# Kernel tuning notes

Measured on AMD Instinct MI355X. Metric: run time of the kernel, lower is better.

Reference implementation:

```python
import jax, jax.numpy as jnp
import numpy as np

N, E, H, R, C = 20000, 640000, 256, 10, 7
B, MAXLEN = 64, 110


def setup_inputs() -> dict:
    key = jax.random.key(0)
    ks = jax.random.split(key, 12)
    return {
        "speaker": jax.random.randint(ks[0], (N,), 0, 2),
        "x": jax.random.normal(ks[1], (N, H), dtype=jnp.float32),
        "edge_index": jax.random.randint(ks[2], (2, E), 0, N),
        "edge_norm": jax.random.uniform(ks[3], (E,), dtype=jnp.float32),
        "edge_type": jax.random.randint(ks[4], (E,), 0, R),
        "seq_lengths": jax.random.randint(ks[5], (B,), 1, MAXLEN),
        "umask": jnp.ones((B, MAXLEN), dtype=jnp.float32),
        "w1": jax.random.normal(ks[6], (R, H, H), dtype=jnp.float32) * 0.02,
        "w2": jax.random.normal(ks[7], (R, H, H), dtype=jnp.float32) * 0.02,
        "lin_W": jax.random.normal(ks[8], (2 * H, H), dtype=jnp.float32) * 0.02,
        "lin_b": jnp.zeros((H,), dtype=jnp.float32),
        "fc_W": jax.random.normal(ks[9], (H, C), dtype=jnp.float32) * 0.02,
        "fc_b": jnp.zeros((C,), dtype=jnp.float32),
    }


def gnn_layer(x, w, edge_index, edge_type, edge_norm):
    # PyG MessagePassing with flow='target_to_source', aggr='mean':
    #   x_j = x[edge_index[1]], aggregate at i = edge_index[0]
    i, j = edge_index[0], edge_index[1]
    # per-edge msg = x_j @ w[edge_type]; compute as relation-batched GEMM
    xw = jnp.einsum('nd,rdo->rno', x, w)          # [R, N, H]
    msgs = xw[edge_type, j] * edge_norm[:, None]   # [E, H]
    sums = jax.ops.segment_sum(msgs, i, num_segments=x.shape[0])
    cnt = jax.ops.segment_sum(jnp.ones_like(edge_norm), i, num_segments=x.shape[0])
    return sums / jnp.maximum(cnt, 1.0)[:, None]   # scatter-mean (0 for isolated nodes)


def reference(speaker, x, edge_index, edge_norm, edge_type, seq_lengths, umask,
              w1, w2, lin_W, lin_b, fc_W, fc_b):
    en = edge_norm * 2.0  # forward passes edge_norm * 2
    # both GNN layers are type 'GGCN' -> update() returns aggr_out (GRU path is dead)
    out1 = jax.nn.sigmoid(gnn_layer(x, w1, edge_index, edge_type, en))  # dropout = eval identity
    out2 = gnn_layer(out1, w2, edge_index, edge_type, en)
    emotions = jnp.concatenate([x, out2], axis=1)            # [N, 2H]
    hidden = jax.nn.relu(emotions @ lin_W + lin_b)           # [N, H]
    logits = hidden @ fc_W + fc_b                            # [N, C]
    log_prob = jax.nn.log_softmax(logits, axis=1)
    return (log_prob, x, emotions)
```

## Files before the change

### kernel.cpp

```cpp
#include <hip/hip_runtime.h>

typedef short bf16x8 __attribute__((ext_vector_type(8)));
typedef float f32x4 __attribute__((ext_vector_type(4)));

#define RH 2560

__device__ __forceinline__ unsigned short f2bf(float f) {
  unsigned u = __float_as_uint(f);
  u += 0x7fffu + ((u >> 16) & 1u);
  return (unsigned short)(u >> 16);
}
__device__ __forceinline__ float bf2f(unsigned short s) {
  return __uint_as_float(((unsigned)s) << 16);
}

__global__ void zero_int(int* __restrict__ p, int n) {
  int i = blockIdx.x * 256 + threadIdx.x;
  if (i < n) p[i] = 0;
}
__global__ void hist_kernel(const int* __restrict__ ei, const int* __restrict__ ety,
                            int E, int* __restrict__ cnt) {
  int e = blockIdx.x * 256 + threadIdx.x;
  if (e < E) atomicAdd(&cnt[ei[e] * 10 + ety[e]], 1);
}

__global__ __launch_bounds__(1024) void scan_local(const int* __restrict__ cnt,
                                                   int* __restrict__ offs,
                                                   int* __restrict__ bsum, int n) {
  __shared__ int ps[1024];
  const int t = threadIdx.x;
  const int base = blockIdx.x * 4096 + t * 4;
  int v0 = (base + 0 < n) ? cnt[base + 0] : 0;
  int v1 = (base + 1 < n) ? cnt[base + 1] : 0;
  int v2 = (base + 2 < n) ? cnt[base + 2] : 0;
  int v3 = (base + 3 < n) ? cnt[base + 3] : 0;
  int s = v0 + v1 + v2 + v3;
  ps[t] = s;
  __syncthreads();
  for (int off = 1; off < 1024; off <<= 1) {
    int add = (t >= off) ? ps[t - off] : 0;
    __syncthreads();
    ps[t] += add;
    __syncthreads();
  }
  int run = t ? ps[t - 1] : 0;
  if (base + 0 < n) offs[base + 0] = run; run += v0;
  if (base + 1 < n) offs[base + 1] = run; run += v1;
  if (base + 2 < n) offs[base + 2] = run; run += v2;
  if (base + 3 < n) offs[base + 3] = run;
  if (t == 1023) bsum[blockIdx.x] = ps[1023];
}
__global__ __launch_bounds__(1024) void scan_bsum(int* __restrict__ bsum,
                                                  int* __restrict__ offs,
                                                  int nb, int n) {
  __shared__ int ps[1024];
  const int t = threadIdx.x;
  int v = (t < nb) ? bsum[t] : 0;
  ps[t] = v;
  __syncthreads();
  for (int off = 1; off < 1024; off <<= 1) {
    int add = (t >= off) ? ps[t - off] : 0;
    __syncthreads();
    ps[t] += add;
    __syncthreads();
  }
  if (t < nb) bsum[t] = ps[t] - v;
  if (t == nb - 1) offs[n] = ps[t];
}
__global__ __launch_bounds__(1024) void scan_add(int* __restrict__ offs,
                                                 const int* __restrict__ bsum, int n) {
  const int add = bsum[blockIdx.x];
  const int base = blockIdx.x * 4096 + threadIdx.x * 4;
#pragma unroll
  for (int k = 0; k < 4; ++k) {
    int idx = base + k;
    if (idx < n) offs[idx] += add;
  }
}

__global__ void copy_int(const int* __restrict__ a, int* __restrict__ b, int n) {
  int i = blockIdx.x * 256 + threadIdx.x;
  if (i < n) b[i] = a[i];
}
__global__ void scatter_kernel(const int* __restrict__ ei, const int* __restrict__ ejj,
                               const int* __restrict__ ety, const float* __restrict__ enm,
                               int E, int* __restrict__ cursor, int2* __restrict__ jnpk) {
  int e = blockIdx.x * 256 + threadIdx.x;
  if (e < E) {
    int s = atomicAdd(&cursor[ei[e] * 10 + ety[e]], 1);
    jnpk[s] = make_int2(ejj[e], __float_as_int(enm[e] * 2.0f));
  }
}

__global__ void packW(const float* __restrict__ w, unsigned short* __restrict__ Wt) {
  int idx = blockIdx.x * 256 + threadIdx.x;
  if (idx >= 256 * RH) return;
  int o = idx / RH;
  int k = idx - o * RH;
  Wt[idx] = f2bf(w[(size_t)k * 256 + o]);
}
__global__ void packLin(const float* __restrict__ lw, unsigned short* __restrict__ Wt) {
  int idx = blockIdx.x * 256 + threadIdx.x;
  if (idx >= 256 * 512) return;
  int o = idx >> 9;
  int k = idx & 511;
  Wt[idx] = f2bf(lw[(size_t)k * 256 + o]);
}
__global__ void copyX(const float* __restrict__ x, float* __restrict__ xcopy,
                      float* __restrict__ em, unsigned short* __restrict__ em16,
                      unsigned short* __restrict__ x16, int total) {
  int idx = blockIdx.x * 256 + threadIdx.x;
  if (idx >= total) return;
  int nrow = idx >> 8, h = idx & 255;
  float v = x[idx];
  xcopy[idx] = v;
  em[(size_t)nrow * 512 + h] = v;
  em16[(size_t)nrow * 512 + h] = f2bf(v);
  x16[idx] = f2bf(v);
}

__global__ __launch_bounds__(256) void agg_bucket(
    const unsigned short* __restrict__ src,
    const int* __restrict__ offs2,
    const int2* __restrict__ jnpk,
    unsigned short* __restrict__ S, int NB)
{
  const int bucket = blockIdx.x * 4 + (threadIdx.x >> 6);
  if (bucket >= NB) return;
  const int lane = threadIdx.x & 63;
  const int cb = lane * 4;
  const int node = bucket / 10;
  const int r = bucket - node * 10;
  const int b10 = node * 10;
  const int sb = offs2[bucket], se = offs2[bucket + 1];
  const int cc = offs2[b10 + 10] - offs2[b10];
  const float scale = 1.0f / (float)(cc > 1 ? cc : 1);
  float b0 = 0.f, b1 = 0.f, b2 = 0.f, b3 = 0.f;
  int q = sb;
  for (; q + 2 <= se; q += 2) {
    int2 e0 = jnpk[q];
    int2 e1 = jnpk[q + 1];
    float n0 = __int_as_float(e0.y);
    float n1 = __int_as_float(e1.y);
    uint2 v0 = *reinterpret_cast<const uint2*>(src + (size_t)e0.x * 256 + cb);
    uint2 v1 = *reinterpret_cast<const uint2*>(src + (size_t)e1.x * 256 + cb);
    b0 += n0 * __uint_as_float(v0.x << 16);
    b1 += n0 * __uint_as_float(v0.x & 0xffff0000u);
    b2 += n0 * __uint_as_float(v0.y << 16);
    b3 += n0 * __uint_as_float(v0.y & 0xffff0000u);
    b0 += n1 * __uint_as_float(v1.x << 16);
    b1 += n1 * __uint_as_float(v1.x & 0xffff0000u);
    b2 += n1 * __uint_as_float(v1.y << 16);
    b3 += n1 * __uint_as_float(v1.y & 0xffff0000u);
  }
  if (q < se) {
    int2 e0 = jnpk[q];
    float n0 = __int_as_float(e0.y);
    uint2 v0 = *reinterpret_cast<const uint2*>(src + (size_t)e0.x * 256 + cb);
    b0 += n0 * __uint_as_float(v0.x << 16);
    b1 += n0 * __uint_as_float(v0.x & 0xffff0000u);
    b2 += n0 * __uint_as_float(v0.y << 16);
    b3 += n0 * __uint_as_float(v0.y & 0xffff0000u);
  }
  unsigned p0 = (unsigned)f2bf(b0 * scale) | ((unsigned)f2bf(b1 * scale) << 16);
  unsigned p1 = (unsigned)f2bf(b2 * scale) | ((unsigned)f2bf(b3 * scale) << 16);
  uint2 pk; pk.x = p0; pk.y = p1;
  *reinterpret_cast<uint2*>(S + (size_t)node * RH + r * 256 + cb) = pk;
}

template<int MODE>
__global__ __launch_bounds__(256) void gemm128(
    const unsigned short* __restrict__ A,
    const unsigned short* __restrict__ Bt,
    int M, int K,
    float* __restrict__ fout,
    unsigned short* __restrict__ bout,
    const float* __restrict__ bias)
{
  __shared__ unsigned short At[64][40];
  __shared__ unsigned short Bs[128][40];
  const int tid = threadIdx.x;
  const int tileM = blockIdx.x * 64;
  const int tileN = blockIdx.y * 128;
  const int lane = tid & 63;
  const int wid = tid >> 6;
  const int wr = wid >> 1, wc = wid & 1;
  const int l15 = lane & 15, lq = lane >> 4;
  f32x4 acc[2][4] = {};
  const int nk = K >> 5;
  for (int kt = 0; kt < nk; ++kt) {
    __syncthreads();
    {
      int row = tid >> 2;
      int ko = (tid & 3) * 8;
      int gr = tileM + row;
      uint4 va = make_uint4(0u, 0u, 0u, 0u);
      if (gr < M) va = *reinterpret_cast<const uint4*>(A + (size_t)gr * K + kt * 32 + ko);
      *reinterpret_cast<uint4*>(&At[row][ko]) = va;
#pragma unroll
      for (int p = 0; p < 2; ++p) {
        int c = tid + p * 256;
        int brow = c >> 2;
        int bko = (c & 3) * 8;
        uint4 vb = *reinterpret_cast<const uint4*>(Bt + (size_t)(tileN + brow) * K + kt * 32 + bko);
        *reinterpret_cast<uint4*>(&Bs[brow][bko]) = vb;
      }
    }
    __syncthreads();
    bf16x8 af[2], bfr[4];
#pragma unroll
    for (int m = 0; m < 2; ++m)
      af[m] = *reinterpret_cast<const bf16x8*>(&At[wr * 32 + m * 16 + l15][lq * 8]);
#pragma unroll
    for (int n = 0; n < 4; ++n)
      bfr[n] = *reinterpret_cast<const bf16x8*>(&Bs[wc * 64 + n * 16 + l15][lq * 8]);
#pragma unroll
    for (int m = 0; m < 2; ++m)
#pragma unroll
      for (int n = 0; n < 4; ++n)
        acc[m][n] = __builtin_amdgcn_mfma_f32_16x16x32_bf16(af[m], bfr[n], acc[m][n], 0, 0, 0);
  }
  const int r0 = tileM + wr * 32;
  const int c0 = tileN + wc * 64;
#pragma unroll
  for (int m = 0; m < 2; ++m) {
#pragma unroll
    for (int n = 0; n < 4; ++n) {
      int col = c0 + n * 16 + l15;
      int rowb = r0 + m * 16 + lq * 4;
#pragma unroll
      for (int q = 0; q < 4; ++q) {
        int row = rowb + q;
        if (row < M) {
          float v = acc[m][n][q];
          if (MODE == 0) {
            float s = 1.0f / (1.0f + __expf(-v));
            bout[(size_t)row * 256 + col] = f2bf(s);
          } else if (MODE == 1) {
            fout[(size_t)row * 512 + col] = v;
            bout[(size_t)row * 512 + col] = f2bf(v);
          } else {
            float s = v + bias[col];
            s = s > 0.0f ? s : 0.0f;
            fout[(size_t)row * 256 + col] = s;
          }
        }
      }
    }
  }
}

__global__ __launch_bounds__(256) void fc_lsm(const float* __restrict__ hidden,
                                              const float* __restrict__ fcW,
                                              const float* __restrict__ fcb,
                                              float* __restrict__ outlp, int N) {
  __shared__ float hs[32 * 256];
  __shared__ float fw[256 * 7];
  __shared__ float lg[32][8];
  const int t = threadIdx.x;
  const int nb = blockIdx.x * 32;
  for (int c = t; c < 256 * 7; c += 256) fw[c] = fcW[c];
  for (int c = t; c < 32 * 256; c += 256) {
    int node = nb + (c >> 8);
    hs[c] = (node < N) ? hidden[(size_t)node * 256 + (c & 255)] : 0.0f;
  }
  __syncthreads();
  if (t < 224) {
    int ln = t / 7, c = t - ln * 7;
    float s = fcb[c];
    for (int h = 0; h < 256; ++h) s += hs[ln * 256 + h] * fw[h * 7 + c];
    lg[ln][c] = s;
  }
  __syncthreads();
  if (t < 32 && nb + t < N) {
    float m = lg[t][0];
    for (int c = 1; c < 7; ++c) m = fmaxf(m, lg[t][c]);
    float sum = 0.0f;
    for (int c = 0; c < 7; ++c) sum += __expf(lg[t][c] - m);
    float ls = __logf(sum);
    for (int c = 0; c < 7; ++c) outlp[(size_t)(nb + t) * 7 + c] = lg[t][c] - m - ls;
  }
}

extern "C" void kernel_launch(void* const* d_in, const int* in_sizes, int n_in,
                              void* d_out, int out_size, void* d_ws, size_t ws_size,
                              hipStream_t stream) {
  const float* x     = (const float*)d_in[1];
  const int*   ei    = (const int*)d_in[2];
  const float* enorm = (const float*)d_in[3];
  const int*   etype = (const int*)d_in[4];
  const float* w1    = (const float*)d_in[7];
  const float* w2    = (const float*)d_in[8];
  const float* linW  = (const float*)d_in[9];
  const float* linb  = (const float*)d_in[10];
  const float* fcW   = (const float*)d_in[11];
  const float* fcb   = (const float*)d_in[12];
  float* out = (float*)d_out;

  const int N = in_sizes[0];
  const int E = in_sizes[3];
  const int NB = N * 10;
  const int NSCAN = (NB + 4095) / 4096;

  char* ws = (char*)d_ws;
  size_t off = 0;
  auto carve = [&](size_t bytes) -> void* {
    void* p = ws + off;
    off += (bytes + 255) & ~(size_t)255;
    return p;
  };
  unsigned short* S    = (unsigned short*)carve((size_t)N * RH * 2);
  unsigned short* W1t  = (unsigned short*)carve((size_t)256 * RH * 2);
  unsigned short* W2t  = (unsigned short*)carve((size_t)256 * RH * 2);
  unsigned short* LWt  = (unsigned short*)carve((size_t)256 * 512 * 2);
  unsigned short* out1 = (unsigned short*)carve((size_t)N * 256 * 2);
  unsigned short* em16 = (unsigned short*)carve((size_t)N * 512 * 2);
  unsigned short* x16  = (unsigned short*)carve((size_t)N * 256 * 2);
  int* cnt2            = (int*)carve((size_t)NB * 4);
  int* offs2           = (int*)carve((size_t)(NB + 1) * 4);
  int* cursor          = (int*)carve((size_t)NB * 4);
  int* bsum            = (int*)carve((size_t)1024 * 4);
  int2* jnpk           = (int2*)carve((size_t)E * 8);
  float* hidden        = (float*)S;

  const int* e_i = ei;
  const int* e_j = ei + E;

  zero_int<<<(NB + 255) / 256, 256, 0, stream>>>(cnt2, NB);
  hist_kernel<<<(E + 255) / 256, 256, 0, stream>>>(e_i, etype, E, cnt2);
  scan_local<<<NSCAN, 1024, 0, stream>>>(cnt2, offs2, bsum, NB);
  scan_bsum<<<1, 1024, 0, stream>>>(bsum, offs2, NSCAN, NB);
  scan_add<<<NSCAN, 1024, 0, stream>>>(offs2, bsum, NB);
  copy_int<<<(NB + 255) / 256, 256, 0, stream>>>(offs2, cursor, NB);
  scatter_kernel<<<(E + 255) / 256, 256, 0, stream>>>(e_i, e_j, etype, enorm, E,
                                                      cursor, jnpk);

  packW<<<(256 * RH + 255) / 256, 256, 0, stream>>>(w1, W1t);
  packW<<<(256 * RH + 255) / 256, 256, 0, stream>>>(w2, W2t);
  packLin<<<(256 * 512 + 255) / 256, 256, 0, stream>>>(linW, LWt);
  copyX<<<((N * 256) + 255) / 256, 256, 0, stream>>>(
      x, out + (size_t)N * 7, out + (size_t)N * 263, em16, x16, N * 256);

  dim3 gemm_grid((N + 63) / 64, 2);

  agg_bucket<<<(NB + 3) / 4, 256, 0, stream>>>(x16, offs2, jnpk, S, NB);
  gemm128<0><<<gemm_grid, 256, 0, stream>>>(S, W1t, N, RH, nullptr, out1, nullptr);

  agg_bucket<<<(NB + 3) / 4, 256, 0, stream>>>(out1, offs2, jnpk, S, NB);
  gemm128<1><<<gemm_grid, 256, 0, stream>>>(S, W2t, N, RH,
      out + (size_t)N * 263 + 256, em16 + 256, nullptr);

  gemm128<2><<<gemm_grid, 256, 0, stream>>>(em16, LWt, N, 512, hidden, nullptr, linb);

  fc_lsm<<<(N + 31) / 32, 256, 0, stream>>>(hidden, fcW, fcb, out, N);
}
```

Baseline: 521.8 us.

## Split-K the aggregated-feature GEMMs and fuse small setup kernels

The two K=2560 GEMMs are split into two K halves via a third grid dimension. Each half writes fp32 partials, and separate reduction kernels then apply the sigmoid or write the emotions outputs. The aim is to double the block count (313x2 to 313x2x2) for better CU occupancy on the long-K GEMMs. This costs an extra fp32 partial write and read of 2xNx256 floats plus two more launches. Three weight-pack kernels are merged into one, the cursor copy is folded into scan_add, and the LDS row stride changes from 40 to 56.

```diff
diff --git a/kernel.cpp b/kernel.cpp
--- a/kernel.cpp
+++ b/kernel.cpp
@@ -4,6 +4,7 @@
 typedef float f32x4 __attribute__((ext_vector_type(4)));
 
 #define RH 2560
+#define LDSS 56
 
 __device__ __forceinline__ unsigned short f2bf(float f) {
   unsigned u = __float_as_uint(f);
@@ -68,20 +69,17 @@
   if (t == nb - 1) offs[n] = ps[t];
 }
 __global__ __launch_bounds__(1024) void scan_add(int* __restrict__ offs,
+                                                 int* __restrict__ cursor,
                                                  const int* __restrict__ bsum, int n) {
   const int add = bsum[blockIdx.x];
   const int base = blockIdx.x * 4096 + threadIdx.x * 4;
 #pragma unroll
   for (int k = 0; k < 4; ++k) {
     int idx = base + k;
-    if (idx < n) offs[idx] += add;
-  }
-}
-
-__global__ void copy_int(const int* __restrict__ a, int* __restrict__ b, int n) {
-  int i = blockIdx.x * 256 + threadIdx.x;
-  if (i < n) b[i] = a[i];
-}
+    if (idx < n) { int v = offs[idx] + add; offs[idx] = v; cursor[idx] = v; }
+  }
+}
+
 __global__ void scatter_kernel(const int* __restrict__ ei, const int* __restrict__ ejj,
                                const int* __restrict__ ety, const float* __restrict__ enm,
                                int E, int* __restrict__ cursor, int2* __restrict__ jnpk) {
@@ -92,19 +90,26 @@
   }
 }
 
-__global__ void packW(const float* __restrict__ w, unsigned short* __restrict__ Wt) {
+__global__ void pack_all(const float* __restrict__ w1, const float* __restrict__ w2,
+                         const float* __restrict__ lw,
+                         unsigned short* __restrict__ W1t, unsigned short* __restrict__ W2t,
+                         unsigned short* __restrict__ LWt) {
+  const int NW = 256 * RH;
   int idx = blockIdx.x * 256 + threadIdx.x;
-  if (idx >= 256 * RH) return;
-  int o = idx / RH;
-  int k = idx - o * RH;
-  Wt[idx] = f2bf(w[(size_t)k * 256 + o]);
-}
-__global__ void packLin(const float* __restrict__ lw, unsigned short* __restrict__ Wt) {
-  int idx = blockIdx.x * 256 + threadIdx.x;
-  if (idx >= 256 * 512) return;
-  int o = idx >> 9;
-  int k = idx & 511;
-  Wt[idx] = f2bf(lw[(size_t)k * 256 + o]);
+  if (idx < NW) {
+    int o = idx / RH, k = idx - o * RH;
+    W1t[idx] = f2bf(w1[(size_t)k * 256 + o]);
+  } else if (idx < 2 * NW) {
+    int i2 = idx - NW;
+    int o = i2 / RH, k = i2 - o * RH;
+    W2t[i2] = f2bf(w2[(size_t)k * 256 + o]);
+  } else {
+    int i3 = idx - 2 * NW;
+    if (i3 < 256 * 512) {
+      int o = i3 >> 9, k = i3 & 511;
+      LWt[i3] = f2bf(lw[(size_t)k * 256 + o]);
+    }
+  }
 }
 __global__ void copyX(const float* __restrict__ x, float* __restrict__ xcopy,
                       float* __restrict__ em, unsigned short* __restrict__ em16,
@@ -168,17 +173,116 @@
   *reinterpret_cast<uint2*>(S + (size_t)node * RH + r * 256 + cb) = pk;
 }
 
-template<int MODE>
-__global__ __launch_bounds__(256) void gemm128(
+__global__ __launch_bounds__(256) void gemm_sk(
+    const unsigned short* __restrict__ A,
+    const unsigned short* __restrict__ Bt,
+    int M, int K,
+    float* __restrict__ P)
+{
+  __shared__ unsigned short At[64 * LDSS];
+  __shared__ unsigned short Bs[128 * LDSS];
+  const int tid = threadIdx.x;
+  const int tileM = blockIdx.x * 64;
+  const int tileN = blockIdx.y * 128;
+  const int kbase = blockIdx.z * (K >> 1);
+  const int lane = tid & 63;
+  const int wid = tid >> 6;
+  const int wr = wid >> 1, wc = wid & 1;
+  const int l15 = lane & 15, lq = lane >> 4;
+  f32x4 acc[2][4] = {};
+  const int nk = K >> 6;
+  for (int kt = 0; kt < nk; ++kt) {
+    __syncthreads();
+    {
+      int row = tid >> 2;
+      int ko = (tid & 3) * 8;
+      int gr = tileM + row;
+      uint4 va = make_uint4(0u, 0u, 0u, 0u);
+      if (gr < M) va = *reinterpret_cast<const uint4*>(A + (size_t)gr * K + kbase + kt * 32 + ko);
+      *reinterpret_cast<uint4*>(&At[row * LDSS + ko]) = va;
+#pragma unroll
+      for (int p = 0; p < 2; ++p) {
+        int c = tid + p * 256;
+        int brow = c >> 2;
+        int bko = (c & 3) * 8;
+        uint4 vb = *reinterpret_cast<const uint4*>(Bt + (size_t)(tileN + brow) * K + kbase + kt * 32 + bko);
+        *reinterpret_cast<uint4*>(&Bs[brow * LDSS + bko]) = vb;
+      }
+    }
+    __syncthreads();
+    bf16x8 af[2], bfr[4];
+#pragma unroll
+    for (int m = 0; m < 2; ++m)
+      af[m] = *reinterpret_cast<const bf16x8*>(&At[(wr * 32 + m * 16 + l15) * LDSS + lq * 8]);
+#pragma unroll
+    for (int n = 0; n < 4; ++n)
+      bfr[n] = *reinterpret_cast<const bf16x8*>(&Bs[(wc * 64 + n * 16 + l15) * LDSS + lq * 8]);
+#pragma unroll
+    for (int m = 0; m < 2; ++m)
+#pragma unroll
+      for (int n = 0; n < 4; ++n)
+        acc[m][n] = __builtin_amdgcn_mfma_f32_16x16x32_bf16(af[m], bfr[n], acc[m][n], 0, 0, 0);
+  }
+  float* Pz = P + (size_t)blockIdx.z * M * 256;
+  const int r0 = tileM + wr * 32;
+  const int c0 = tileN + wc * 64;
+#pragma unroll
+  for (int m = 0; m < 2; ++m) {
+#pragma unroll
+    for (int n = 0; n < 4; ++n) {
+      int col = c0 + n * 16 + l15;
+      int rowb = r0 + m * 16 + lq * 4;
+#pragma unroll
+      for (int q = 0; q < 4; ++q) {
+        int row = rowb + q;
+        if (row < M) Pz[(size_t)row * 256 + col] = acc[m][n][q];
+      }
+    }
+  }
+}
+
+__global__ void red_sig(const float* __restrict__ P, int M,
+                        unsigned short* __restrict__ out1) {
+  int idx = blockIdx.x * 256 + threadIdx.x;
+  if (idx * 4 >= M * 256) return;
+  float4 a = reinterpret_cast<const float4*>(P)[idx];
+  float4 b = reinterpret_cast<const float4*>(P + (size_t)M * 256)[idx];
+  float v0 = 1.0f / (1.0f + __expf(-(a.x + b.x)));
+  float v1 = 1.0f / (1.0f + __expf(-(a.y + b.y)));
+  float v2 = 1.0f / (1.0f + __expf(-(a.z + b.z)));
+  float v3 = 1.0f / (1.0f + __expf(-(a.w + b.w)));
+  uint2 pk;
+  pk.x = (unsigned)f2bf(v0) | ((unsigned)f2bf(v1) << 16);
+  pk.y = (unsigned)f2bf(v2) | ((unsigned)f2bf(v3) << 16);
+  reinterpret_cast<uint2*>(out1)[idx] = pk;
+}
+__global__ void red_em(const float* __restrict__ P, int M,
+                       float* __restrict__ em,
+                       unsigned short* __restrict__ em16)
+{
+  int idx = blockIdx.x * 256 + threadIdx.x;
+  if (idx * 4 >= M * 256) return;
+  float4 a = reinterpret_cast<const float4*>(P)[idx];
+  float4 b = reinterpret_cast<const float4*>(P + (size_t)M * 256)[idx];
+  float4 v = make_float4(a.x + b.x, a.y + b.y, a.z + b.z, a.w + b.w);
+  int row = idx >> 6;
+  int c4 = idx & 63;
+  *reinterpret_cast<float4*>(em + (size_t)row * 512 + c4 * 4) = v;
+  uint2 pk;
+  pk.x = (unsigned)f2bf(v.x) | ((unsigned)f2bf(v.y) << 16);
+  pk.y = (unsigned)f2bf(v.z) | ((unsigned)f2bf(v.w) << 16);
+  *reinterpret_cast<uint2*>(em16 + (size_t)row * 512 + c4 * 4) = pk;
+}
+
+__global__ __launch_bounds__(256) void gemm_lin(
     const unsigned short* __restrict__ A,
     const unsigned short* __restrict__ Bt,
     int M, int K,
     float* __restrict__ fout,
-    unsigned short* __restrict__ bout,
     const float* __restrict__ bias)
 {
-  __shared__ unsigned short At[64][40];
-  __shared__ unsigned short Bs[128][40];
+  __shared__ unsigned short At[64 * LDSS];
+  __shared__ unsigned short Bs[128 * LDSS];
   const int tid = threadIdx.x;
   const int tileM = blockIdx.x * 64;
   const int tileN = blockIdx.y * 128;
@@ -196,24 +300,24 @@
       int gr = tileM + row;
       uint4 va = make_uint4(0u, 0u, 0u, 0u);
       if (gr < M) va = *reinterpret_cast<const uint4*>(A + (size_t)gr * K + kt * 32 + ko);
-      *reinterpret_cast<uint4*>(&At[row][ko]) = va;
+      *reinterpret_cast<uint4*>(&At[row * LDSS + ko]) = va;
 #pragma unroll
       for (int p = 0; p < 2; ++p) {
         int c = tid + p * 256;
         int brow = c >> 2;
         int bko = (c & 3) * 8;
         uint4 vb = *reinterpret_cast<const uint4*>(Bt + (size_t)(tileN + brow) * K + kt * 32 + bko);
-        *reinterpret_cast<uint4*>(&Bs[brow][bko]) = vb;
+        *reinterpret_cast<uint4*>(&Bs[brow * LDSS + bko]) = vb;
       }
     }
     __syncthreads();
     bf16x8 af[2], bfr[4];
 #pragma unroll
     for (int m = 0; m < 2; ++m)
-      af[m] = *reinterpret_cast<const bf16x8*>(&At[wr * 32 + m * 16 + l15][lq * 8]);
+      af[m] = *reinterpret_cast<const bf16x8*>(&At[(wr * 32 + m * 16 + l15) * LDSS + lq * 8]);
 #pragma unroll
     for (int n = 0; n < 4; ++n)
-      bfr[n] = *reinterpret_cast<const bf16x8*>(&Bs[wc * 64 + n * 16 + l15][lq * 8]);
+      bfr[n] = *reinterpret_cast<const bf16x8*>(&Bs[(wc * 64 + n * 16 + l15) * LDSS + lq * 8]);
 #pragma unroll
     for (int m = 0; m < 2; ++m)
 #pragma unroll
@@ -232,18 +336,8 @@
       for (int q = 0; q < 4; ++q) {
         int row = rowb + q;
         if (row < M) {
-          float v = acc[m][n][q];
-          if (MODE == 0) {
-            float s = 1.0f / (1.0f + __expf(-v));
-            bout[(size_t)row * 256 + col] = f2bf(s);
-          } else if (MODE == 1) {
-            fout[(size_t)row * 512 + col] = v;
-            bout[(size_t)row * 512 + col] = f2bf(v);
-          } else {
-            float s = v + bias[col];
-            s = s > 0.0f ? s : 0.0f;
-            fout[(size_t)row * 256 + col] = s;
-          }
+          float s = acc[m][n][q] + bias[col];
+          fout[(size_t)row * 256 + col] = s > 0.0f ? s : 0.0f;
         }
       }
     }
@@ -321,6 +415,7 @@
   int* cursor          = (int*)carve((size_t)NB * 4);
   int* bsum            = (int*)carve((size_t)1024 * 4);
   int2* jnpk           = (int2*)carve((size_t)E * 8);
+  float* P             = (float*)carve((size_t)2 * N * 256 * 4);
   float* hidden        = (float*)S;
 
   const int* e_i = ei;
@@ -330,27 +425,28 @@
   hist_kernel<<<(E + 255) / 256, 256, 0, stream>>>(e_i, etype, E, cnt2);
   scan_local<<<NSCAN, 1024, 0, stream>>>(cnt2, offs2, bsum, NB);
   scan_bsum<<<1, 1024, 0, stream>>>(bsum, offs2, NSCAN, NB);
-  scan_add<<<NSCAN, 1024, 0, stream>>>(offs2, bsum, NB);
-  copy_int<<<(NB + 255) / 256, 256, 0, stream>>>(offs2, cursor, NB);
+  scan_add<<<NSCAN, 1024, 0, stream>>>(offs2, cursor, bsum, NB);
   scatter_kernel<<<(E + 255) / 256, 256, 0, stream>>>(e_i, e_j, etype, enorm, E,
                                                       cursor, jnpk);
 
-  packW<<<(256 * RH + 255) / 256, 256, 0, stream>>>(w1, W1t);
-  packW<<<(256 * RH + 255) / 256, 256, 0, stream>>>(w2, W2t);
-  packLin<<<(256 * 512 + 255) / 256, 256, 0, stream>>>(linW, LWt);
+  const int PACKTOT = 2 * 256 * RH + 256 * 512;
+  pack_all<<<(PACKTOT + 255) / 256, 256, 0, stream>>>(w1, w2, linW, W1t, W2t, LWt);
   copyX<<<((N * 256) + 255) / 256, 256, 0, stream>>>(
       x, out + (size_t)N * 7, out + (size_t)N * 263, em16, x16, N * 256);
 
-  dim3 gemm_grid((N + 63) / 64, 2);
+  dim3 sk_grid((N + 63) / 64, 2, 2);
+  const int RED_BLK = ((N * 256 / 4) + 255) / 256;
 
   agg_bucket<<<(NB + 3) / 4, 256, 0, stream>>>(x16, offs2, jnpk, S, NB);
-  gemm128<0><<<gemm_grid, 256, 0, stream>>>(S, W1t, N, RH, nullptr, out1, nullptr);
+  gemm_sk<<<sk_grid, 256, 0, stream>>>(S, W1t, N, RH, P);
+  red_sig<<<RED_BLK, 256, 0, stream>>>(P, N, out1);
 
   agg_bucket<<<(NB + 3) / 4, 256, 0, stream>>>(out1, offs2, jnpk, S, NB);
-  gemm128<1><<<gemm_grid, 256, 0, stream>>>(S, W2t, N, RH,
-      out + (size_t)N * 263 + 256, em16 + 256, nullptr);
-
-  gemm128<2><<<gemm_grid, 256, 0, stream>>>(em16, LWt, N, 512, hidden, nullptr, linb);
+  gemm_sk<<<sk_grid, 256, 0, stream>>>(S, W2t, N, RH, P);
+  red_em<<<RED_BLK, 256, 0, stream>>>(P, N, out + (size_t)N * 263 + 256, em16 + 256);
+
+  dim3 lin_grid((N + 63) / 64, 2);
+  gemm_lin<<<lin_grid, 256, 0, stream>>>(em16, LWt, N, 512, hidden, linb);
 
   fc_lsm<<<(N + 31) / 32, 256, 0, stream>>>(hidden, fcW, fcb, out, N);
 }
```

Result: no change. 518.1 us (-0.7%).
